# Performance work log

Hardware: AMD Instinct MI355X
Metric: run time of the kernel (lower is better)

## Reference

```python
import jax, jax.numpy as jnp
import numpy as np

K = 16          # patch_size
P2 = 256        # patch_size**2
D_PD = 512      # learned base dictionary atoms (D_out_lam_pd)
D_LAM = 112     # adaptive atoms from sdict, = 8*14 (D_out_lam)
DD = D_PD + D_LAM  # 624
T = 5
INDICE = 112
MIN_V, MAX_V = 0.0, 1.0


def _idx(H, W, k, stride):
    oh = (H - k) // stride + 1
    ow = (W - k) // stride + 1
    r = jnp.arange(k)[:, None] + stride * jnp.arange(oh)[None, :]  # [k, oh]
    c = jnp.arange(k)[:, None] + stride * jnp.arange(ow)[None, :]  # [k, ow]
    return r[:, None, :, None], c[None, :, None, :], oh, ow


def _unfold(x, k, stride):
    # torch.nn.Unfold: [N, C*k*k, L] with (C, kh, kw) channel order, row-major L
    N, C, H, W = x.shape
    r, c, oh, ow = _idx(H, W, k, stride)
    return x[:, :, r, c].reshape(N, C * k * k, oh * ow)


def _fold(p, H, W, k):
    # torch.nn.functional.fold (col2im) with stride 1, overlap-add
    N, ckk, L = p.shape
    r, c, oh, ow = _idx(H, W, k, 1)
    C = ckk // (k * k)
    out = jnp.zeros((N, C, H, W), p.dtype)
    return out.at[:, :, r, c].add(p.reshape(N, C, k, k, oh, ow))


def _mlp(x, ws):
    # Linear + clamp(min=0) chain, no relu after last layer (dropout = eval identity)
    for w, b in ws[:-1]:
        x = jnp.maximum(x @ w + b, 0.0)
    w, b = ws[-1]
    return x @ w + b


def _cbam(x, w1, w2, conv_w):
    # standard CBAM: channel attention (shared MLP on avg+max pool) then 7x7 spatial attention
    def mlp(v):
        return jnp.maximum(v @ w1, 0.0) @ w2
    ca = jax.nn.sigmoid(mlp(x.mean(axis=(2, 3))) + mlp(x.max(axis=(2, 3))))
    x = x * ca[:, :, None, None]
    s = jnp.stack([x.mean(axis=1), x.max(axis=1)], axis=1)  # [N,2,h,w]
    sa = jax.lax.conv_general_dilated(s, conv_w, (1, 1), [(3, 3), (3, 3)],
                                      dimension_numbers=('NCHW', 'OIHW', 'NCHW'))
    return x * jax.nn.sigmoid(sa)


def _soft(x, l):
    return jnp.sign(x) * jnp.maximum(jnp.abs(x) - l, 0.0)


def _stage(img, Dict, c, sd_ws, ca1, ca2, saw, lam_ws, pd_ws, w_ws):
    N, C, H, W = img.shape
    uf = _unfold(img, K, 1).transpose(0, 2, 1)     # [N, L, 256]
    uf1 = _unfold(img, K, 8).transpose(0, 2, 1)    # [N, L1, 256]
    step = uf1.shape[1] // INDICE                  # static under jit
    ext = uf1[:, ::step, :][:, :INDICE, :]         # [N, 112, 256]
    sd = _mlp(ext, sd_ws)                          # linears1..4
    sd = sd / jnp.maximum(jnp.linalg.norm(sd, axis=-1, keepdims=True), 1e-12)
    sd = _cbam(sd.transpose(0, 2, 1).reshape(N, P2, 8, 14), ca1, ca2, saw)
    sd = sd.reshape(N, P2, INDICE)                 # [N, 256, 112]
    Dcat = jnp.concatenate([jnp.broadcast_to(Dict, (N,) + Dict.shape), sd], axis=-1)  # [N,256,624]
    # thresholds: l = cat(lpd, ls)
    thr = jnp.concatenate([_mlp(uf, pd_ws) / c, _mlp(uf, lam_ws) / c], axis=-1)  # [N,L,624]
    y = uf @ Dcat                                  # [N, L, 624]
    # S = (I - D^T D / c)^T; D^T D is symmetric so the transpose is a no-op
    S = jnp.eye(DD, dtype=img.dtype) - (Dcat.transpose(0, 2, 1) @ Dcat) / c
    z = _soft(y, thr)
    for _ in range(T):  # LISTA unrolled iterations (T static)
        z = _soft(z @ S + y / c, thr)
    Wg = jax.nn.sigmoid(_mlp(uf, w_ws))            # [N, L, 256]
    x_pred = jnp.clip(z @ Dcat.transpose(0, 2, 1), MIN_V, MAX_V) * Wg
    num = _fold(x_pred.transpose(0, 2, 1), H, W, K)
    den = _fold(Wg.transpose(0, 2, 1), H, W, K)    # fold of W * ones
    return num / den


def _forward(x, Dict, c, s1w, s1b, s2w, s2b, s3w, s3b, s4w, s4b, caw1, caw2, saw,
             a1w, a1b, a2w, a2b, a3w, a3b, p1w, p1b, p2w, p2b, p3w, p3b,
             b1w, b1b, b2w, b2b, b3w, b3b, q1w, q1b, q2w, q2b, q3w, q3b,
             w1w, w1b, w2w, w2b, w3w, w3b):
    sd_ws = [(s1w, s1b), (s2w, s2b), (s3w, s3b), (s4w, s4b)]
    w_ws = [(w1w, w1b), (w2w, w2b), (w3w, w3b)]
    res = _stage(x, Dict, c, sd_ws, caw1, caw2, saw,
                 [(a1w, a1b), (a2w, a2b), (a3w, a3b)],
                 [(p1w, p1b), (p2w, p2b), (p3w, p3b)], w_ws)
    res = _stage(res, Dict, c, sd_ws, caw1, caw2, saw,
                 [(b1w, b1b), (b2w, b2b), (b3w, b3b)],
                 [(q1w, q1b), (q2w, q2b), (q3w, q3b)], w_ws)
    return res


def setup_inputs() -> dict:
    key = jax.random.key(0)
    ks = iter(jax.random.split(key, 40))
    d = {}
    d['x'] = jax.random.uniform(next(ks), (2, 1, 128, 128), jnp.float32)
    Dm = jax.random.normal(next(ks), (P2, D_PD), jnp.float32)
    d['Dict'] = Dm / jnp.linalg.norm(Dm, axis=0, keepdims=True)  # unit-norm atoms
    d['c'] = jnp.asarray(10.0, jnp.float32)  # c > ||D^T D||_2
    dims = {'s1': (256, 512), 's2': (512, 1024), 's3': (1024, 512), 's4': (512, 256),
            'a1': (256, 1024), 'a2': (1024, 512), 'a3': (512, 112),
            'p1': (256, 1024), 'p2': (1024, 512), 'p3': (512, 512),
            'b1': (256, 1024), 'b2': (1024, 512), 'b3': (512, 112),
            'q1': (256, 1024), 'q2': (1024, 512), 'q3': (512, 512),
            'w1': (256, 1024), 'w2': (1024, 512), 'w3': (512, 256)}
    for name, (i, o) in dims.items():
        d[name + 'w'] = jax.random.normal(next(ks), (i, o), jnp.float32) / np.float32(np.sqrt(i))
        d[name + 'b'] = jnp.zeros((o,), jnp.float32)
    d['caw1'] = jax.random.normal(next(ks), (256, 512), jnp.float32) / np.float32(16.0)
    d['caw2'] = jax.random.normal(next(ks), (512, 256), jnp.float32) / np.float32(np.sqrt(512))
    d['saw'] = jax.random.normal(next(ks), (1, 2, 7, 7), jnp.float32) * np.float32(0.1)
    return d


def reference(x, Dict, c, s1w, s1b, s2w, s2b, s3w, s3b, s4w, s4b, caw1, caw2, saw,
              a1w, a1b, a2w, a2b, a3w, a3b, p1w, p1b, p2w, p2b, p3w, p3b,
              b1w, b1b, b2w, b2b, b3w, b3b, q1w, q1b, q2w, q2b, q3w, q3b,
              w1w, w1b, w2w, w2b, w3w, w3b):
    return _forward(x, Dict, c, s1w, s1b, s2w, s2b, s3w, s3b, s4w, s4b, caw1, caw2, saw,
                    a1w, a1b, a2w, a2b, a3w, a3b, p1w, p1b, p2w, p2b, p3w, p3b,
                    b1w, b1b, b2w, b2b, b3w, b3b, q1w, q1b, q2w, q2b, q3w, q3b,
                    w1w, w1b, w2w, w2b, w3w, w3b)
```

## Files before the change

### kernel.cpp

```cpp
#include <hip/hip_runtime.h>
#include <hip/hip_bf16.h>
#include <math.h>

#define L_LOC 12769
#define NB 2
#define NLR (NB * L_LOC)
#define NW 20

typedef short short8v __attribute__((ext_vector_type(8)));
typedef float f32x4 __attribute__((ext_vector_type(4)));
typedef __hip_bfloat16 bf16;

__device__ __forceinline__ float softf(float x, float l) {
  float a = fmaxf(fabsf(x) - l, 0.0f);
  return x > 0.0f ? a : (x < 0.0f ? -a : 0.0f);
}
__device__ __forceinline__ float sigf(float x) { return 1.0f / (1.0f + expf(-x)); }
__device__ __forceinline__ void split2(float v, bf16& h, bf16& l) {
  h = __float2bfloat16(v);
  l = __float2bfloat16(v - __bfloat162float(h));
}

enum { ME_RELU = 0, ME_SCALE = 1, ME_SIG = 2, ME_Y = 3, ME_SOFT = 4, ME_XP = 5,
       ME_SMAT = 6, ME_LIN = 7 };

template <int EPI, int TERMS, int WLO>
__global__ __launch_bounds__(256) void mgemm_k(
    const bf16* __restrict__ A, int lda, size_t aOff,
    const bf16* __restrict__ B0, const bf16* __restrict__ B1, int ldb, size_t bOff,
    void* __restrict__ Cv, int ldc, size_t cOff,
    bf16* __restrict__ Zp,
    const float* __restrict__ bias,
    const float* __restrict__ E1, const float* __restrict__ E2, int lde,
    const float* __restrict__ cptr, int bRow, int Rc, int r0, int N, int K)
{
  const int NPA = (TERMS >= 3) ? 2 : 1;
  const int NPB = (TERMS >= 2) ? 2 : 1;
  __shared__ char As[(TERMS >= 3) ? 2 : 1][8192];
  __shared__ char Bs[(TERMS >= 2) ? 2 : 1][8192];
  const int t = threadIdx.x;
  const int lane = t & 63, wv = t >> 6;
  const int wr = wv >> 1, wc = wv & 1;
  const int m0 = blockIdx.x * 128, n0 = blockIdx.y * 128;
  const int nb = (m0 >= bRow) ? 1 : 0;
  const bf16* __restrict__ Bt = nb ? B1 : B0;
  const int row16 = lane & 15, kg = lane >> 4;
  const int grow = t >> 2;
  const int gcol = (t & 3) * 8;
  f32x4 acc[4][4];
#pragma unroll
  for (int i = 0; i < 4; ++i)
#pragma unroll
    for (int j = 0; j < 4; ++j) { acc[i][j][0] = 0.f; acc[i][j][1] = 0.f; acc[i][j][2] = 0.f; acc[i][j][3] = 0.f; }

  for (int k0 = 0; k0 < K; k0 += 32) {
#pragma unroll
    for (int h = 0; h < NPA; ++h)
#pragma unroll
      for (int i = 0; i < 2; ++i) {
        const bf16* ga = A + h * aOff + (size_t)(m0 + i * 64 + grow) * lda + k0 + gcol;
        __builtin_amdgcn_global_load_lds(
            (const __attribute__((address_space(1))) void*)ga,
            (__attribute__((address_space(3))) void*)(As[h] + i * 4096 + wv * 1024), 16, 0, 0);
      }
#pragma unroll
    for (int h = 0; h < NPB; ++h)
#pragma unroll
      for (int i = 0; i < 2; ++i) {
        const bf16* gb = Bt + h * bOff + (size_t)(n0 + i * 64 + grow) * ldb + k0 + gcol;
        __builtin_amdgcn_global_load_lds(
            (const __attribute__((address_space(1))) void*)gb,
            (__attribute__((address_space(3))) void*)(Bs[h] + i * 4096 + wv * 1024), 16, 0, 0);
      }
    __syncthreads();
    short8v ah[4], al[4], bh[4], bl[4];
#pragma unroll
    for (int mi = 0; mi < 4; ++mi) {
      int o = (wr * 64 + mi * 16 + row16) * 64 + kg * 16;
      ah[mi] = *(const short8v*)(As[0] + o);
      if (TERMS >= 3) al[mi] = *(const short8v*)(As[NPA - 1] + o);
    }
#pragma unroll
    for (int ni = 0; ni < 4; ++ni) {
      int o = (wc * 64 + ni * 16 + row16) * 64 + kg * 16;
      bh[ni] = *(const short8v*)(Bs[0] + o);
      if (TERMS >= 2) bl[ni] = *(const short8v*)(Bs[NPB - 1] + o);
    }
#pragma unroll
    for (int mi = 0; mi < 4; ++mi)
#pragma unroll
      for (int ni = 0; ni < 4; ++ni) {
        if (TERMS >= 2)
          acc[mi][ni] = __builtin_amdgcn_mfma_f32_16x16x32_bf16(ah[mi], bl[ni], acc[mi][ni], 0, 0, 0);
        if (TERMS >= 3)
          acc[mi][ni] = __builtin_amdgcn_mfma_f32_16x16x32_bf16(al[mi], bh[ni], acc[mi][ni], 0, 0, 0);
        acc[mi][ni] = __builtin_amdgcn_mfma_f32_16x16x32_bf16(ah[mi], bh[ni], acc[mi][ni], 0, 0, 0);
      }
    __syncthreads();
  }

  float invc = 1.0f;
  if (EPI == ME_SCALE || EPI == ME_SOFT || EPI == ME_SMAT) invc = 1.0f / cptr[0];
  bf16* Cb = (bf16*)Cv;
  float* Cf = (float*)Cv;
#pragma unroll
  for (int ni = 0; ni < 4; ++ni) {
    int col = n0 + wc * 64 + ni * 16 + row16;
    const bool colok = col < N;
    float bv = 0.0f;
    if ((EPI == ME_RELU || EPI == ME_SCALE || EPI == ME_SIG || EPI == ME_LIN) && colok)
      bv = bias[col];
#pragma unroll
    for (int mi = 0; mi < 4; ++mi) {
      int rowb = m0 + wr * 64 + mi * 16 + kg * 4;
#pragma unroll
      for (int r = 0; r < 4; ++r) {
        int row = rowb + r;
        float v = acc[mi][ni][r];
        if (EPI == ME_RELU) {
          if (colok) {
            float o = fmaxf(v + bv, 0.0f);
            size_t ci = (size_t)row * ldc + col;
            if (WLO) {
              bf16 h, l; split2(o, h, l);
              Cb[ci] = h; Cb[ci + cOff] = l;
            } else {
              Cb[ci] = __float2bfloat16(o);
            }
          }
        } else if (EPI == ME_LIN) {
          if (colok && row < Rc) Cf[(size_t)row * ldc + col] = v + bv;
        } else if (EPI == ME_SCALE) {
          if (colok) Cf[(size_t)row * ldc + col] = (v + bv) * invc;
        } else if (EPI == ME_SIG) {
          if (colok) {
            int rl = row - nb * bRow;
            if (rl < Rc && rl >= 0)
              Cf[(size_t)col * NLR + (size_t)nb * L_LOC + r0 + rl] = sigf(v + bv);
          }
        } else if (EPI == ME_Y) {
          if (colok) {
            size_t e = (size_t)row * lde + col;
            Cf[(size_t)row * ldc + col] = v;
            Zp[(size_t)row * 640 + col] = __float2bfloat16(softf(v, E1[e]));
          }
        } else if (EPI == ME_SOFT) {
          if (colok) {
            size_t e = (size_t)row * lde + col;
            Cb[(size_t)row * ldc + col] = __float2bfloat16(softf(v + E1[e] * invc, E2[e]));
          }
        } else if (EPI == ME_XP) {
          int rl = row - nb * bRow;
          if (colok && rl < Rc && rl >= 0) {
            size_t g = (size_t)col * NLR + (size_t)nb * L_LOC + r0 + rl;
            Cf[g] = fminf(fmaxf(v, 0.0f), 1.0f) * E1[g];
          }
        } else {
          float o = (row < 624 && col < 624) ? ((row == col ? 1.0f : 0.0f) - v * invc) : 0.0f;
          bf16 h, l; split2(o, h, l);
          size_t ci = (size_t)row * ldc + col;
          Cb[ci] = h; Cb[ci + cOff] = l;
        }
      }
    }
  }
}

static void mgemm(hipStream_t st, int EPI, int terms, int wlo,
                  const bf16* A, int lda, size_t aOff,
                  const bf16* B0, const bf16* B1, int ldb, size_t bOff,
                  void* C, int ldc, size_t cOff,
                  bf16* Zp,
                  const float* bias, const float* E1, const float* E2, int lde,
                  const float* cptr, int bRow, int Rc, int r0,
                  int Mp, int N, int K)
{
  dim3 grid(Mp / 128, (N + 127) / 128), blk(256);
#define MG(ep, tm, wl) mgemm_k<ep, tm, wl><<<grid, blk, 0, st>>>(A, lda, aOff, B0, B1, ldb, bOff, C, ldc, cOff, Zp, bias, E1, E2, lde, cptr, bRow, Rc, r0, N, K)
  if (EPI == ME_RELU && terms == 1 && !wlo) { MG(ME_RELU, 1, 0); }
  else if (EPI == ME_RELU && terms == 1)    { MG(ME_RELU, 1, 1); }
  else if (EPI == ME_RELU)                  { MG(ME_RELU, 3, 1); }
  else if (EPI == ME_LIN)                   { MG(ME_LIN, 3, 0); }
  else if (EPI == ME_SCALE)                 { MG(ME_SCALE, 3, 0); }
  else if (EPI == ME_SIG)                   { MG(ME_SIG, 1, 0); }
  else if (EPI == ME_Y)                     { MG(ME_Y, 3, 0); }
  else if (EPI == ME_SOFT)                  { MG(ME_SOFT, 2, 0); }
  else if (EPI == ME_XP)                    { MG(ME_XP, 2, 0); }
  else                                      { MG(ME_SMAT, 3, 0); }
#undef MG
}

struct WTable {
  const float* src[NW];
  bf16* dst[NW];
  int K[NW], N[NW], Kp[NW], Np[NW];
  long long loOff[NW];
  int base[NW + 1];
};

__global__ void wtransall_k(WTable w) {
  int idx = blockIdx.x * 256 + threadIdx.x;
  if (idx >= w.base[NW]) return;
  int s = 0;
  while (s < NW - 1 && idx >= w.base[s + 1]) ++s;
  int li = idx - w.base[s];
  int Kp = w.Kp[s];
  int n = li / Kp, k = li - n * Kp;
  float v = (n < w.N[s] && k < w.K[s]) ? w.src[s][(size_t)k * w.N[s] + n] : 0.0f;
  bf16 h, l; split2(v, h, l);
  w.dst[s][li] = h;
  w.dst[s][li + w.loOff[s]] = l;
}

__global__ void biascat_k(const float* p1, const float* a1, const float* w1b,
                          const float* q1, const float* b1,
                          float* c1, float* c2) {
  int i = blockIdx.x * 256 + threadIdx.x;
  if (i >= 3072) return;
  int br = i >> 10, o = i & 1023;
  c1[i] = br == 0 ? p1[o] : (br == 1 ? a1[o] : w1b[o]);
  c2[i] = br == 0 ? q1[o] : (br == 1 ? b1[o] : w1b[o]);
}

__global__ void extb_k(const float* __restrict__ img, bf16* __restrict__ dst) {
  int idx = blockIdx.x * 256 + threadIdx.x;
  int row = idx >> 8, p = idx & 255;
  float v = 0.0f;
  if (row < 224) {
    int n = row / 112, e = row - n * 112;
    int l1 = 2 * e, i1 = l1 / 15, j1 = l1 - i1 * 15;
    v = img[n * 16384 + (8 * i1 + (p >> 4)) * 128 + 8 * j1 + (p & 15)];
  }
  bf16 h, l; split2(v, h, l);
  dst[idx] = h; dst[idx + 65536] = l;
}

__global__ void rownorm224_k(float* sd) {
  int r = blockIdx.x, t = threadIdx.x;
  float v[4], s = 0.0f;
#pragma unroll
  for (int j = 0; j < 4; ++j) { v[j] = sd[r * 256 + t + 64 * j]; s += v[j] * v[j]; }
#pragma unroll
  for (int o = 1; o < 64; o <<= 1) s += __shfl_xor(s, o);
  float sc = 1.0f / fmaxf(sqrtf(s), 1e-12f);
#pragma unroll
  for (int j = 0; j < 4; ++j) sd[r * 256 + t + 64 * j] = v[j] * sc;
}

__global__ void dcatconv_k(const float* __restrict__ Dict, const float* __restrict__ Dc,
                           bf16* __restrict__ Db, bf16* __restrict__ DbT) {
  int idx = blockIdx.x * 256 + threadIdx.x;
  if (idx >= 327680) return;
  int n = idx / 163840, r = idx - n * 163840;
  int p = r / 640, a = r - p * 640;
  float v = 0.0f;
  if (a < 512)      v = Dict[p * 512 + a];
  else if (a < 624) v = Dc[(size_t)n * 159744 + p * 624 + a];
  bf16 h, l; split2(v, h, l);
  size_t base = (size_t)n * 327680;
  Db[base + p * 640 + a] = h;
  Db[base + 163840 + p * 640 + a] = l;
  DbT[base + (size_t)a * 256 + p] = h;
  DbT[base + 163840 + (size_t)a * 256 + p] = l;
}

__global__ void unfold_k(const float* __restrict__ img, bf16* __restrict__ uf,
                         int r0, int Rc, int bRowc, size_t pOff) {
  int bi = blockIdx.x;
  int nb = bi >= Rc;
  int rl = nb ? bi - Rc : bi;
  int row = nb * bRowc + rl;
  int p = threadIdx.x;
  int l = r0 + rl;
  int i0 = l / 113, j0 = l - i0 * 113;
  float v = img[nb * 16384 + (i0 + (p >> 4)) * 128 + j0 + (p & 15)];
  bf16 h, lo; split2(v, h, lo);
  size_t o = (size_t)row * 256 + p;
  uf[o] = h; uf[o + pOff] = lo;
}

__global__ __launch_bounds__(1024) void cbam_k(
    const float* __restrict__ sd, const float* __restrict__ w1,
    const float* __restrict__ w2, const float* __restrict__ saw,
    float* __restrict__ Dcat)
{
  __shared__ float mv[512], xv[512], hm[1024], hx[1024], ca[512];
  __shared__ float smean[224], smax[224];
  const int t = threadIdx.x;
  if (t < 512) {
    int n = t >> 8, ch = t & 255;
    float s = 0.0f, m = -INFINITY;
    for (int e = 0; e < 112; ++e) {
      float v = sd[(n * 112 + e) * 256 + ch];
      s += v; m = fmaxf(m, v);
    }
    mv[t] = s * (1.0f / 112.0f);
    xv[t] = m;
  }
  __syncthreads();
  {
    int n = t >> 9, o = t & 511;
    float sm = 0.0f, sx = 0.0f;
    for (int i = 0; i < 256; ++i) {
      float w = w1[i * 512 + o];
      sm += mv[n * 256 + i] * w;
      sx += xv[n * 256 + i] * w;
    }
    hm[t] = fmaxf(sm, 0.0f);
    hx[t] = fmaxf(sx, 0.0f);
  }
  __syncthreads();
  if (t < 512) {
    int n = t >> 8, ch = t & 255;
    float s = 0.0f;
    for (int o = 0; o < 512; ++o) s += (hm[n * 512 + o] + hx[n * 512 + o]) * w2[o * 256 + ch];
    ca[t] = sigf(s);
  }
  __syncthreads();
  if (t < 224) {
    int n = t / 112, s = t % 112;
    float sum = 0.0f, mx = -INFINITY;
    for (int ch = 0; ch < 256; ++ch) {
      float v = sd[(n * 112 + s) * 256 + ch] * ca[n * 256 + ch];
      Dcat[(size_t)n * 159744 + ch * 624 + 512 + s] = v;
      sum += v; mx = fmaxf(mx, v);
    }
    smean[t] = sum * (1.0f / 256.0f);
    smax[t] = mx;
  }
  __syncthreads();
  if (t < 224) {
    int n = t / 112, s = t % 112;
    int h = s / 14, w = s % 14;
    float acc = 0.0f;
    for (int dh = 0; dh < 7; ++dh) {
      int hh = h + dh - 3; if (hh < 0 || hh >= 8) continue;
      for (int dw = 0; dw < 7; ++dw) {
        int ww = w + dw - 3; if (ww < 0 || ww >= 14) continue;
        int sp = hh * 14 + ww;
        acc += smean[n * 112 + sp] * saw[dh * 7 + dw] + smax[n * 112 + sp] * saw[49 + dh * 7 + dw];
      }
    }
    float sg = sigf(acc);
    for (int ch = 0; ch < 256; ++ch) Dcat[(size_t)n * 159744 + ch * 624 + 512 + s] *= sg;
  }
}

__global__ void folddiv_k(const float* __restrict__ xpT, const float* __restrict__ wgT,
                          float* __restrict__ out) {
  int idx = blockIdx.x * 256 + threadIdx.x;
  if (idx >= 32768) return;
  int n = idx >> 14, rem = idx & 16383;
  int i = rem >> 7, j = rem & 127;
  float num = 0.0f, den = 0.0f;
  int kh0 = (i - 112 > 0) ? i - 112 : 0;
  int kh1 = (i < 15) ? i : 15;
  int kw0 = (j - 112 > 0) ? j - 112 : 0;
  int kw1 = (j < 15) ? j : 15;
  for (int kh = kh0; kh <= kh1; ++kh)
    for (int kw = kw0; kw <= kw1; ++kw) {
      int l = (i - kh) * 113 + (j - kw);
      size_t base = (size_t)(kh * 16 + kw) * NLR + (size_t)n * L_LOC + l;
      num += xpT[base];
      den += wgT[base];
    }
  out[idx] = num / den;
}

struct Bufs {
  float *xp, *wg, *Dcat_f, *sd, *res;
  bf16 *Db, *DbT, *Sb;
  bf16 *extb, *sdh1, *sdh2, *sdh3;
  bf16 *uf, *h1, *h2, *z, *zn;
  float *thr, *y;
  size_t ufO, h2O;
  int R;
};

static void run_stage(hipStream_t st, const float* const* in, const float* img,
                      float* outimg, int pd0, int lam0,
                      const bf16* Wcat, const float* bcat,
                      bf16* const* WtPd, bf16* const* WtLam, bf16* const* WtW,
                      bf16* const* Ws, const Bufs& b)
{
  const float* cptr = in[2];
  const int BIG = 1 << 30;
  extb_k<<<dim3(256), dim3(256), 0, st>>>(img, b.extb);
  mgemm(st, ME_RELU, 3, 1, b.extb, 256, 65536, Ws[0], Ws[0], 256, 512 * 256,
        b.sdh1, 512, 256 * 512, 0, in[4], 0, 0, 0, cptr, BIG, 224, 0, 256, 512, 256);
  mgemm(st, ME_RELU, 3, 1, b.sdh1, 512, 256 * 512, Ws[1], Ws[1], 512, 1024 * 512,
        b.sdh2, 1024, 256 * 1024, 0, in[6], 0, 0, 0, cptr, BIG, 224, 0, 256, 1024, 512);
  mgemm(st, ME_RELU, 3, 1, b.sdh2, 1024, 256 * 1024, Ws[2], Ws[2], 1024, 512 * 1024,
        b.sdh3, 512, 256 * 512, 0, in[8], 0, 0, 0, cptr, BIG, 224, 0, 256, 512, 1024);
  mgemm(st, ME_LIN, 3, 0, b.sdh3, 512, 256 * 512, Ws[3], Ws[3], 512, 256 * 512,
        b.sd, 256, 0, 0, in[10], 0, 0, 0, cptr, BIG, 224, 0, 256, 256, 512);
  rownorm224_k<<<dim3(224), dim3(64), 0, st>>>(b.sd);
  cbam_k<<<dim3(1), dim3(1024), 0, st>>>(b.sd, in[41], in[42], in[43], b.Dcat_f);
  dcatconv_k<<<dim3(1280), dim3(256), 0, st>>>(in[1], b.Dcat_f, b.Db, b.DbT);
  for (int n = 0; n < NB; ++n) {
    const bf16* Dt = b.DbT + (size_t)n * 327680;
    mgemm(st, ME_SMAT, 3, 0, Dt, 256, 163840, Dt, Dt, 256, 163840,
          b.Sb + (size_t)n * 819200, 640, 409600, 0,
          0, 0, 0, 0, cptr, BIG, 624, 0, 640, 640, 256);
  }

  for (int r0 = 0; r0 < L_LOC; r0 += b.R) {
    int Rc = L_LOC - r0; if (Rc > b.R) Rc = b.R;
    int bRowc = ((Rc + 127) / 128) * 128;
    int Mp = 2 * bRowc;
    unfold_k<<<dim3(2 * Rc), dim3(256), 0, st>>>(img, b.uf, r0, Rc, bRowc, b.ufO);
    mgemm(st, ME_RELU, 1, 0, b.uf, 256, b.ufO, Wcat, Wcat, 256, 3072 * 256,
          b.h1, 3072, 0, 0, bcat, 0, 0, 0, cptr, bRowc, Rc, r0, Mp, 3072, 256);
    mgemm(st, ME_RELU, 1, 1, b.h1, 3072, 0, WtPd[1], WtPd[1], 1024, 512 * 1024,
          b.h2, 512, b.h2O, 0, in[pd0 + 3], 0, 0, 0, cptr, bRowc, Rc, r0, Mp, 512, 1024);
    mgemm(st, ME_SCALE, 3, 0, b.h2, 512, b.h2O, WtPd[2], WtPd[2], 512, 512 * 512,
          b.thr, 640, 0, 0, in[pd0 + 5], 0, 0, 0, cptr, bRowc, Rc, r0, Mp, 512, 512);
    mgemm(st, ME_RELU, 1, 1, b.h1 + 1024, 3072, 0, WtLam[1], WtLam[1], 1024, 512 * 1024,
          b.h2, 512, b.h2O, 0, in[lam0 + 3], 0, 0, 0, cptr, bRowc, Rc, r0, Mp, 512, 1024);
    mgemm(st, ME_SCALE, 3, 0, b.h2, 512, b.h2O, WtLam[2], WtLam[2], 512, 128 * 512,
          b.thr + 512, 640, 0, 0, in[lam0 + 5], 0, 0, 0, cptr, bRowc, Rc, r0, Mp, 112, 512);
    mgemm(st, ME_RELU, 1, 1, b.h1 + 2048, 3072, 0, WtW[1], WtW[1], 1024, 512 * 1024,
          b.h2, 512, b.h2O, 0, in[38], 0, 0, 0, cptr, bRowc, Rc, r0, Mp, 512, 1024);
    mgemm(st, ME_SIG, 1, 0, b.h2, 512, b.h2O, WtW[2], WtW[2], 512, 256 * 512,
          b.wg, 0, 0, 0, in[40], 0, 0, 0, cptr, bRowc, Rc, r0, Mp, 256, 512);
    mgemm(st, ME_Y, 3, 0, b.uf, 256, b.ufO, b.DbT, b.DbT + 327680, 256, 163840,
          b.y, 640, 0, b.z, 0, b.thr, 0, 640, cptr, bRowc, Rc, r0, Mp, 624, 256);
    bf16* zi = b.z; bf16* zo = b.zn;
    for (int it = 0; it < 5; ++it) {
      mgemm(st, ME_SOFT, 2, 0, zi, 640, 0, b.Sb, b.Sb + 819200, 640, 409600,
            zo, 640, 0, 0, 0, b.y, b.thr, 640, cptr, bRowc, Rc, r0, Mp, 624, 640);
      bf16* tmp = zi; zi = zo; zo = tmp;
    }
    mgemm(st, ME_XP, 2, 0, zi, 640, 0, b.Db, b.Db + 327680, 640, 163840,
          b.xp, 0, 0, 0, 0, b.wg, 0, 0, cptr, bRowc, Rc, r0, Mp, 256, 640);
  }
  folddiv_k<<<dim3(128), dim3(256), 0, st>>>(b.xp, b.wg, outimg);
}

extern "C" void kernel_launch(void* const* d_in, const int* in_sizes, int n_in,
                              void* d_out, int out_size, void* d_ws, size_t ws_size,
                              hipStream_t stream)
{
  (void)in_sizes; (void)n_in; (void)out_size;
  const float* const* in = (const float* const*)d_in;
  char* base = (char*)d_ws;
  size_t off = 0;
  auto allocf = [&](size_t nelem) -> float* {
    float* p = (float*)(base + off);
    off += ((nelem * 4 + 255) / 256) * 256;
    return p;
  };
  auto allocb2 = [&](size_t nelem) -> bf16* {
    bf16* p = (bf16*)(base + off);
    off += ((nelem * 2 * 2 + 255) / 256) * 256;
    return p;
  };
  auto allocb1 = [&](size_t nelem) -> bf16* {
    bf16* p = (bf16*)(base + off);
    off += ((nelem * 2 + 255) / 256) * 256;
    return p;
  };
  Bufs b;
  b.xp = allocf((size_t)NLR * 256);
  b.wg = allocf((size_t)NLR * 256);
  b.Dcat_f = allocf(2 * 256 * 624);
  b.sd = allocf(224 * 256);
  b.res = allocf(2 * 16384);
  b.Db = allocb2(2 * 163840);
  b.DbT = allocb2(2 * 163840);
  b.Sb = allocb2(2 * 409600);
  b.extb = allocb2(256 * 256);
  b.sdh1 = allocb2(256 * 512);
  b.sdh2 = allocb2(256 * 1024);
  b.sdh3 = allocb2(256 * 512);
  bf16* Wcat1 = allocb1(2 * 3072 * 256);
  bf16* Wcat2 = allocb1(2 * 3072 * 256);
  float* bcat1 = allocf(3072);
  float* bcat2 = allocf(3072);

  bf16 *Wa[3], *Wp[3], *Wb[3], *Wq[3], *Ww[3], *Ws[4];
  WTable wt;
  int ne = 0, tot = 0;
  auto addw = [&](const float* src, bf16* dst, int K, int N, int Kp, int Np, long long loOff) {
    wt.src[ne] = src; wt.dst[ne] = dst;
    wt.K[ne] = K; wt.N[ne] = N; wt.Kp[ne] = Kp; wt.Np[ne] = Np;
    wt.loOff[ne] = loOff; wt.base[ne] = tot;
    tot += Np * Kp; ++ne;
  };
  int sdK[4] = {256, 512, 1024, 512}, sdN[4] = {512, 1024, 512, 256}, sdIdx[4] = {3, 5, 7, 9};
  for (int i = 0; i < 4; ++i) {
    Ws[i] = allocb2((size_t)sdN[i] * sdK[i]);
    addw(in[sdIdx[i]], Ws[i], sdK[i], sdN[i], sdK[i], sdN[i], (long long)sdN[i] * sdK[i]);
  }
  struct WD { bf16** slot; int idx, K, N, Kp, Np; };
  WD wd[10] = {
    {&Wa[1], 13, 1024, 512, 1024, 512}, {&Wa[2], 15, 512, 112, 512, 128},
    {&Wp[1], 19, 1024, 512, 1024, 512}, {&Wp[2], 21, 512, 512, 512, 512},
    {&Wb[1], 25, 1024, 512, 1024, 512}, {&Wb[2], 27, 512, 112, 512, 128},
    {&Wq[1], 31, 1024, 512, 1024, 512}, {&Wq[2], 33, 512, 512, 512, 512},
    {&Ww[1], 37, 1024, 512, 1024, 512}, {&Ww[2], 39, 512, 256, 512, 256},
  };
  for (int i = 0; i < 10; ++i) {
    *wd[i].slot = allocb2((size_t)wd[i].Np * wd[i].Kp);
    addw(in[wd[i].idx], *wd[i].slot, wd[i].K, wd[i].N, wd[i].Kp, wd[i].Np,
         (long long)wd[i].Np * wd[i].Kp);
  }
  const long long catLo = 3072LL * 256;
  addw(in[17], Wcat1 + 0 * 262144, 256, 1024, 256, 1024, catLo);
  addw(in[11], Wcat1 + 1 * 262144, 256, 1024, 256, 1024, catLo);
  addw(in[35], Wcat1 + 2 * 262144, 256, 1024, 256, 1024, catLo);
  addw(in[29], Wcat2 + 0 * 262144, 256, 1024, 256, 1024, catLo);
  addw(in[23], Wcat2 + 1 * 262144, 256, 1024, 256, 1024, catLo);
  addw(in[35], Wcat2 + 2 * 262144, 256, 1024, 256, 1024, catLo);
  wt.base[NW] = tot;
  wtransall_k<<<dim3((tot + 255) / 256), dim3(256), 0, stream>>>(wt);
  biascat_k<<<dim3(12), dim3(256), 0, stream>>>(in[18], in[12], in[36], in[30], in[24],
                                                bcat1, bcat2);

  long long avail = (long long)ws_size - (long long)off - (1 << 20);
  long long perrow2 = 2LL * (16896 + 64);
  int R = 12800;
  if (avail / perrow2 < 12800) R = (int)(avail / perrow2);
  R &= ~127;
  if (R < 128) R = 128;
  b.R = R;
  size_t rows2 = (size_t)2 * R;
  b.uf = allocb2(rows2 * 256);  b.ufO = rows2 * 256;
  b.h1 = allocb1(rows2 * 3072);
  b.h2 = allocb2(rows2 * 512);  b.h2O = rows2 * 512;
  b.z = allocb1(rows2 * 640);
  b.zn = allocb1(rows2 * 640);
  b.thr = allocf(rows2 * 640);
  b.y = allocf(rows2 * 640);

  run_stage(stream, in, in[0], b.res, 17, 11, Wcat1, bcat1, Wp, Wa, Ww, Ws, b);
  run_stage(stream, in, b.res, (float*)d_out, 29, 23, Wcat2, bcat2, Wq, Wb, Ww, Ws, b);
}
```

Measured before the change: 3.845 ms.

## Split CBAM into multi-block kernels and unfuse first-layer branch GEMMs

The single-block 1024-thread CBAM kernel becomes four small kernels (mean/max, hidden MLP, channel attention output, spatial attention), each spread over several blocks so the tiny MLP no longer runs serially on one CU. The concatenated 3072-wide first-layer GEMM shared by the three branches is replaced by three separate 1024-wide GEMMs, each followed by its consumer, which shrinks the h1 buffer and removes the bias-concatenation kernel. The trade is more kernel launches and three passes over the unfolded input instead of one, in exchange for a smaller working set and better CU utilisation in CBAM.

```diff
diff --git a/kernel.cpp b/kernel.cpp
--- a/kernel.cpp
+++ b/kernel.cpp
@@ -5,7 +5,7 @@
 #define L_LOC 12769
 #define NB 2
 #define NLR (NB * L_LOC)
-#define NW 20
+#define NW 19
 
 typedef short short8v __attribute__((ext_vector_type(8)));
 typedef float f32x4 __attribute__((ext_vector_type(4)));
@@ -212,16 +212,6 @@
   w.dst[s][li + w.loOff[s]] = l;
 }
 
-__global__ void biascat_k(const float* p1, const float* a1, const float* w1b,
-                          const float* q1, const float* b1,
-                          float* c1, float* c2) {
-  int i = blockIdx.x * 256 + threadIdx.x;
-  if (i >= 3072) return;
-  int br = i >> 10, o = i & 1023;
-  c1[i] = br == 0 ? p1[o] : (br == 1 ? a1[o] : w1b[o]);
-  c2[i] = br == 0 ? q1[o] : (br == 1 ? b1[o] : w1b[o]);
-}
-
 __global__ void extb_k(const float* __restrict__ img, bf16* __restrict__ dst) {
   int idx = blockIdx.x * 256 + threadIdx.x;
   int row = idx >> 8, p = idx & 255;
@@ -245,6 +235,75 @@
   float sc = 1.0f / fmaxf(sqrtf(s), 1e-12f);
 #pragma unroll
   for (int j = 0; j < 4; ++j) sd[r * 256 + t + 64 * j] = v[j] * sc;
+}
+
+__global__ void meanmax_k(const float* __restrict__ sd, float* mv, float* xv) {
+  int id = blockIdx.x * 256 + threadIdx.x;
+  int n = id >> 8, ch = id & 255;
+  float s = 0.0f, m = -INFINITY;
+  for (int e = 0; e < 112; ++e) {
+    float v = sd[(n * 112 + e) * 256 + ch];
+    s += v; m = fmaxf(m, v);
+  }
+  mv[id] = s * (1.0f / 112.0f);
+  xv[id] = m;
+}
+
+__global__ void cah_k(const float* __restrict__ mv, const float* __restrict__ xv,
+                      const float* __restrict__ w1, float* hm, float* hx) {
+  int id = blockIdx.x * 256 + threadIdx.x;
+  int n = id >> 9, o = id & 511;
+  float sm = 0.0f, sx = 0.0f;
+#pragma unroll 4
+  for (int i = 0; i < 256; ++i) {
+    float w = w1[i * 512 + o];
+    sm = fmaf(mv[n * 256 + i], w, sm);
+    sx = fmaf(xv[n * 256 + i], w, sx);
+  }
+  hm[id] = fmaxf(sm, 0.0f);
+  hx[id] = fmaxf(sx, 0.0f);
+}
+
+__global__ void cao_k(const float* __restrict__ hm, const float* __restrict__ hx,
+                      const float* __restrict__ w2, float* ca) {
+  int id = blockIdx.x * 256 + threadIdx.x;
+  int n = id >> 8, ch = id & 255;
+  float s = 0.0f;
+#pragma unroll 4
+  for (int o = 0; o < 512; ++o)
+    s = fmaf(hm[n * 512 + o] + hx[n * 512 + o], w2[o * 256 + ch], s);
+  ca[id] = sigf(s);
+}
+
+__global__ void spatial_k(const float* __restrict__ sd, const float* __restrict__ ca,
+                          const float* __restrict__ saw, float* __restrict__ Dcat) {
+  __shared__ float smean[112], smax[112];
+  const int n = blockIdx.x, t = threadIdx.x;
+  if (t < 112) {
+    float sum = 0.0f, mx = -INFINITY;
+    for (int ch = 0; ch < 256; ++ch) {
+      float v = sd[(n * 112 + t) * 256 + ch] * ca[n * 256 + ch];
+      Dcat[(size_t)n * 159744 + ch * 624 + 512 + t] = v;
+      sum += v; mx = fmaxf(mx, v);
+    }
+    smean[t] = sum * (1.0f / 256.0f);
+    smax[t] = mx;
+  }
+  __syncthreads();
+  if (t < 112) {
+    int h = t / 14, w = t % 14;
+    float acc = 0.0f;
+    for (int dh = 0; dh < 7; ++dh) {
+      int hh = h + dh - 3; if (hh < 0 || hh >= 8) continue;
+      for (int dw = 0; dw < 7; ++dw) {
+        int ww = w + dw - 3; if (ww < 0 || ww >= 14) continue;
+        int sp = hh * 14 + ww;
+        acc += smean[sp] * saw[dh * 7 + dw] + smax[sp] * saw[49 + dh * 7 + dw];
+      }
+    }
+    float sg = sigf(acc);
+    for (int ch = 0; ch < 256; ++ch) Dcat[(size_t)n * 159744 + ch * 624 + 512 + t] *= sg;
+  }
 }
 
 __global__ void dcatconv_k(const float* __restrict__ Dict, const float* __restrict__ Dc,
@@ -277,73 +336,6 @@
   bf16 h, lo; split2(v, h, lo);
   size_t o = (size_t)row * 256 + p;
   uf[o] = h; uf[o + pOff] = lo;
-}
-
-__global__ __launch_bounds__(1024) void cbam_k(
-    const float* __restrict__ sd, const float* __restrict__ w1,
-    const float* __restrict__ w2, const float* __restrict__ saw,
-    float* __restrict__ Dcat)
-{
-  __shared__ float mv[512], xv[512], hm[1024], hx[1024], ca[512];
-  __shared__ float smean[224], smax[224];
-  const int t = threadIdx.x;
-  if (t < 512) {
-    int n = t >> 8, ch = t & 255;
-    float s = 0.0f, m = -INFINITY;
-    for (int e = 0; e < 112; ++e) {
-      float v = sd[(n * 112 + e) * 256 + ch];
-      s += v; m = fmaxf(m, v);
-    }
-    mv[t] = s * (1.0f / 112.0f);
-    xv[t] = m;
-  }
-  __syncthreads();
-  {
-    int n = t >> 9, o = t & 511;
-    float sm = 0.0f, sx = 0.0f;
-    for (int i = 0; i < 256; ++i) {
-      float w = w1[i * 512 + o];
-      sm += mv[n * 256 + i] * w;
-      sx += xv[n * 256 + i] * w;
-    }
-    hm[t] = fmaxf(sm, 0.0f);
-    hx[t] = fmaxf(sx, 0.0f);
-  }
-  __syncthreads();
-  if (t < 512) {
-    int n = t >> 8, ch = t & 255;
-    float s = 0.0f;
-    for (int o = 0; o < 512; ++o) s += (hm[n * 512 + o] + hx[n * 512 + o]) * w2[o * 256 + ch];
-    ca[t] = sigf(s);
-  }
-  __syncthreads();
-  if (t < 224) {
-    int n = t / 112, s = t % 112;
-    float sum = 0.0f, mx = -INFINITY;
-    for (int ch = 0; ch < 256; ++ch) {
-      float v = sd[(n * 112 + s) * 256 + ch] * ca[n * 256 + ch];
-      Dcat[(size_t)n * 159744 + ch * 624 + 512 + s] = v;
-      sum += v; mx = fmaxf(mx, v);
-    }
-    smean[t] = sum * (1.0f / 256.0f);
-    smax[t] = mx;
-  }
-  __syncthreads();
-  if (t < 224) {
-    int n = t / 112, s = t % 112;
-    int h = s / 14, w = s % 14;
-    float acc = 0.0f;
-    for (int dh = 0; dh < 7; ++dh) {
-      int hh = h + dh - 3; if (hh < 0 || hh >= 8) continue;
-      for (int dw = 0; dw < 7; ++dw) {
-        int ww = w + dw - 3; if (ww < 0 || ww >= 14) continue;
-        int sp = hh * 14 + ww;
-        acc += smean[n * 112 + sp] * saw[dh * 7 + dw] + smax[n * 112 + sp] * saw[49 + dh * 7 + dw];
-      }
-    }
-    float sg = sigf(acc);
-    for (int ch = 0; ch < 256; ++ch) Dcat[(size_t)n * 159744 + ch * 624 + 512 + s] *= sg;
-  }
 }
 
 __global__ void folddiv_k(const float* __restrict__ xpT, const float* __restrict__ wgT,
@@ -369,6 +361,7 @@
 
 struct Bufs {
   float *xp, *wg, *Dcat_f, *sd, *res;
+  float *mv, *xv, *hm, *hx, *ca;
   bf16 *Db, *DbT, *Sb;
   bf16 *extb, *sdh1, *sdh2, *sdh3;
   bf16 *uf, *h1, *h2, *z, *zn;
@@ -379,7 +372,6 @@
 
 static void run_stage(hipStream_t st, const float* const* in, const float* img,
                       float* outimg, int pd0, int lam0,
-                      const bf16* Wcat, const float* bcat,
                       bf16* const* WtPd, bf16* const* WtLam, bf16* const* WtW,
                       bf16* const* Ws, const Bufs& b)
 {
@@ -395,7 +387,10 @@
   mgemm(st, ME_LIN, 3, 0, b.sdh3, 512, 256 * 512, Ws[3], Ws[3], 512, 256 * 512,
         b.sd, 256, 0, 0, in[10], 0, 0, 0, cptr, BIG, 224, 0, 256, 256, 512);
   rownorm224_k<<<dim3(224), dim3(64), 0, st>>>(b.sd);
-  cbam_k<<<dim3(1), dim3(1024), 0, st>>>(b.sd, in[41], in[42], in[43], b.Dcat_f);
+  meanmax_k<<<dim3(2), dim3(256), 0, st>>>(b.sd, b.mv, b.xv);
+  cah_k<<<dim3(4), dim3(256), 0, st>>>(b.mv, b.xv, in[41], b.hm, b.hx);
+  cao_k<<<dim3(2), dim3(256), 0, st>>>(b.hm, b.hx, in[42], b.ca);
+  spatial_k<<<dim3(2), dim3(128), 0, st>>>(b.sd, b.ca, in[43], b.Dcat_f);
   dcatconv_k<<<dim3(1280), dim3(256), 0, st>>>(in[1], b.Dcat_f, b.Db, b.DbT);
   for (int n = 0; n < NB; ++n) {
     const bf16* Dt = b.DbT + (size_t)n * 327680;
@@ -409,17 +404,21 @@
     int bRowc = ((Rc + 127) / 128) * 128;
     int Mp = 2 * bRowc;
     unfold_k<<<dim3(2 * Rc), dim3(256), 0, st>>>(img, b.uf, r0, Rc, bRowc, b.ufO);
-    mgemm(st, ME_RELU, 1, 0, b.uf, 256, b.ufO, Wcat, Wcat, 256, 3072 * 256,
-          b.h1, 3072, 0, 0, bcat, 0, 0, 0, cptr, bRowc, Rc, r0, Mp, 3072, 256);
-    mgemm(st, ME_RELU, 1, 1, b.h1, 3072, 0, WtPd[1], WtPd[1], 1024, 512 * 1024,
+    mgemm(st, ME_RELU, 1, 0, b.uf, 256, b.ufO, WtPd[0], WtPd[0], 256, 1024 * 256,
+          b.h1, 1024, 0, 0, in[pd0 + 1], 0, 0, 0, cptr, bRowc, Rc, r0, Mp, 1024, 256);
+    mgemm(st, ME_RELU, 1, 1, b.h1, 1024, 0, WtPd[1], WtPd[1], 1024, 512 * 1024,
           b.h2, 512, b.h2O, 0, in[pd0 + 3], 0, 0, 0, cptr, bRowc, Rc, r0, Mp, 512, 1024);
     mgemm(st, ME_SCALE, 3, 0, b.h2, 512, b.h2O, WtPd[2], WtPd[2], 512, 512 * 512,
           b.thr, 640, 0, 0, in[pd0 + 5], 0, 0, 0, cptr, bRowc, Rc, r0, Mp, 512, 512);
-    mgemm(st, ME_RELU, 1, 1, b.h1 + 1024, 3072, 0, WtLam[1], WtLam[1], 1024, 512 * 1024,
+    mgemm(st, ME_RELU, 1, 0, b.uf, 256, b.ufO, WtLam[0], WtLam[0], 256, 1024 * 256,
+          b.h1, 1024, 0, 0, in[lam0 + 1], 0, 0, 0, cptr, bRowc, Rc, r0, Mp, 1024, 256);
+    mgemm(st, ME_RELU, 1, 1, b.h1, 1024, 0, WtLam[1], WtLam[1], 1024, 512 * 1024,
           b.h2, 512, b.h2O, 0, in[lam0 + 3], 0, 0, 0, cptr, bRowc, Rc, r0, Mp, 512, 1024);
     mgemm(st, ME_SCALE, 3, 0, b.h2, 512, b.h2O, WtLam[2], WtLam[2], 512, 128 * 512,
           b.thr + 512, 640, 0, 0, in[lam0 + 5], 0, 0, 0, cptr, bRowc, Rc, r0, Mp, 112, 512);
-    mgemm(st, ME_RELU, 1, 1, b.h1 + 2048, 3072, 0, WtW[1], WtW[1], 1024, 512 * 1024,
+    mgemm(st, ME_RELU, 1, 0, b.uf, 256, b.ufO, WtW[0], WtW[0], 256, 1024 * 256,
+          b.h1, 1024, 0, 0, in[36], 0, 0, 0, cptr, bRowc, Rc, r0, Mp, 1024, 256);
+    mgemm(st, ME_RELU, 1, 1, b.h1, 1024, 0, WtW[1], WtW[1], 1024, 512 * 1024,
           b.h2, 512, b.h2O, 0, in[38], 0, 0, 0, cptr, bRowc, Rc, r0, Mp, 512, 1024);
     mgemm(st, ME_SIG, 1, 0, b.h2, 512, b.h2O, WtW[2], WtW[2], 512, 256 * 512,
           b.wg, 0, 0, 0, in[40], 0, 0, 0, cptr, bRowc, Rc, r0, Mp, 256, 512);
@@ -466,6 +465,9 @@
   b.Dcat_f = allocf(2 * 256 * 624);
   b.sd = allocf(224 * 256);
   b.res = allocf(2 * 16384);
+  b.mv = allocf(512); b.xv = allocf(512);
+  b.hm = allocf(1024); b.hx = allocf(1024);
+  b.ca = allocf(512);
   b.Db = allocb2(2 * 163840);
   b.DbT = allocb2(2 * 163840);
   b.Sb = allocb2(2 * 409600);
@@ -473,52 +475,38 @@
   b.sdh1 = allocb2(256 * 512);
   b.sdh2 = allocb2(256 * 1024);
   b.sdh3 = allocb2(256 * 512);
-  bf16* Wcat1 = allocb1(2 * 3072 * 256);
-  bf16* Wcat2 = allocb1(2 * 3072 * 256);
-  float* bcat1 = allocf(3072);
-  float* bcat2 = allocf(3072);
 
   bf16 *Wa[3], *Wp[3], *Wb[3], *Wq[3], *Ww[3], *Ws[4];
   WTable wt;
   int ne = 0, tot = 0;
-  auto addw = [&](const float* src, bf16* dst, int K, int N, int Kp, int Np, long long loOff) {
+  auto addw = [&](const float* src, bf16* dst, int K, int N, int Kp, int Np) {
     wt.src[ne] = src; wt.dst[ne] = dst;
     wt.K[ne] = K; wt.N[ne] = N; wt.Kp[ne] = Kp; wt.Np[ne] = Np;
-    wt.loOff[ne] = loOff; wt.base[ne] = tot;
+    wt.loOff[ne] = (long long)Np * Kp; wt.base[ne] = tot;
     tot += Np * Kp; ++ne;
   };
   int sdK[4] = {256, 512, 1024, 512}, sdN[4] = {512, 1024, 512, 256}, sdIdx[4] = {3, 5, 7, 9};
   for (int i = 0; i < 4; ++i) {
     Ws[i] = allocb2((size_t)sdN[i] * sdK[i]);
-    addw(in[sdIdx[i]], Ws[i], sdK[i], sdN[i], sdK[i], sdN[i], (long long)sdN[i] * sdK[i]);
+    addw(in[sdIdx[i]], Ws[i], sdK[i], sdN[i], sdK[i], sdN[i]);
   }
   struct WD { bf16** slot; int idx, K, N, Kp, Np; };
-  WD wd[10] = {
-    {&Wa[1], 13, 1024, 512, 1024, 512}, {&Wa[2], 15, 512, 112, 512, 128},
-    {&Wp[1], 19, 1024, 512, 1024, 512}, {&Wp[2], 21, 512, 512, 512, 512},
-    {&Wb[1], 25, 1024, 512, 1024, 512}, {&Wb[2], 27, 512, 112, 512, 128},
-    {&Wq[1], 31, 1024, 512, 1024, 512}, {&Wq[2], 33, 512, 512, 512, 512},
-    {&Ww[1], 37, 1024, 512, 1024, 512}, {&Ww[2], 39, 512, 256, 512, 256},
+  WD wd[15] = {
+    {&Wa[0], 11, 256, 1024, 256, 1024}, {&Wa[1], 13, 1024, 512, 1024, 512}, {&Wa[2], 15, 512, 112, 512, 128},
+    {&Wp[0], 17, 256, 1024, 256, 1024}, {&Wp[1], 19, 1024, 512, 1024, 512}, {&Wp[2], 21, 512, 512, 512, 512},
+    {&Wb[0], 23, 256, 1024, 256, 1024}, {&Wb[1], 25, 1024, 512, 1024, 512}, {&Wb[2], 27, 512, 112, 512, 128},
+    {&Wq[0], 29, 256, 1024, 256, 1024}, {&Wq[1], 31, 1024, 512, 1024, 512}, {&Wq[2], 33, 512, 512, 512, 512},
+    {&Ww[0], 35, 256, 1024, 256, 1024}, {&Ww[1], 37, 1024, 512, 1024, 512}, {&Ww[2], 39, 512, 256, 512, 256},
   };
-  for (int i = 0; i < 10; ++i) {
+  for (int i = 0; i < 15; ++i) {
     *wd[i].slot = allocb2((size_t)wd[i].Np * wd[i].Kp);
-    addw(in[wd[i].idx], *wd[i].slot, wd[i].K, wd[i].N, wd[i].Kp, wd[i].Np,
-         (long long)wd[i].Np * wd[i].Kp);
-  }
-  const long long catLo = 3072LL * 256;
-  addw(in[17], Wcat1 + 0 * 262144, 256, 1024, 256, 1024, catLo);
-  addw(in[11], Wcat1 + 1 * 262144, 256, 1024, 256, 1024, catLo);
-  addw(in[35], Wcat1 + 2 * 262144, 256, 1024, 256, 1024, catLo);
-  addw(in[29], Wcat2 + 0 * 262144, 256, 1024, 256, 1024, catLo);
-  addw(in[23], Wcat2 + 1 * 262144, 256, 1024, 256, 1024, catLo);
-  addw(in[35], Wcat2 + 2 * 262144, 256, 1024, 256, 1024, catLo);
+    addw(in[wd[i].idx], *wd[i].slot, wd[i].K, wd[i].N, wd[i].Kp, wd[i].Np);
+  }
   wt.base[NW] = tot;
   wtransall_k<<<dim3((tot + 255) / 256), dim3(256), 0, stream>>>(wt);
-  biascat_k<<<dim3(12), dim3(256), 0, stream>>>(in[18], in[12], in[36], in[30], in[24],
-                                                bcat1, bcat2);
 
   long long avail = (long long)ws_size - (long long)off - (1 << 20);
-  long long perrow2 = 2LL * (16896 + 64);
+  long long perrow2 = 2LL * (12800 + 64);
   int R = 12800;
   if (avail / perrow2 < 12800) R = (int)(avail / perrow2);
   R &= ~127;
@@ -526,13 +514,13 @@
   b.R = R;
   size_t rows2 = (size_t)2 * R;
   b.uf = allocb2(rows2 * 256);  b.ufO = rows2 * 256;
-  b.h1 = allocb1(rows2 * 3072);
+  b.h1 = allocb1(rows2 * 1024);
   b.h2 = allocb2(rows2 * 512);  b.h2O = rows2 * 512;
   b.z = allocb1(rows2 * 640);
   b.zn = allocb1(rows2 * 640);
   b.thr = allocf(rows2 * 640);
   b.y = allocf(rows2 * 640);
 
-  run_stage(stream, in, in[0], b.res, 17, 11, Wcat1, bcat1, Wp, Wa, Ww, Ws, b);
-  run_stage(stream, in, b.res, (float*)d_out, 29, 23, Wcat2, bcat2, Wq, Wb, Ww, Ws, b);
-}
+  run_stage(stream, in, in[0], b.res, 17, 11, Wp, Wa, Ww, Ws, b);
+  run_stage(stream, in, b.res, (float*)d_out, 29, 23, Wq, Wb, Ww, Ws, b);
+}
```

Result: faster. 3.189 ms (-17.1%).
